# Kernel tuning notes

Measured on AMD Instinct MI355X. Metric: run time of the kernel, lower is better.

Reference implementation:

```python
import jax, jax.numpy as jnp
import numpy as np

B, T, W = 64, 64, 20
VIDEO_DIM = 1024
JOINT_DIM = 1024
K, STRIDE = 4, 4
MARGIN = 0.2
EPS = 1e-8


def _l2norm(x, axis=-1):
    n = jnp.sqrt(jnp.sum(x * x, axis=axis, keepdims=True))
    return x / jnp.maximum(n, EPS)


def _conv1d(x, w, b, stride):
    # x: (B, C, L), w: (O, I, K) -> (B, O, L_out), VALID padding (padding=0)
    y = jax.lax.conv_general_dilated(x, w, (stride,), 'VALID',
                                     dimension_numbers=('NCH', 'OIH', 'NCH'))
    return y + b[None, :, None]


def _diag_loss(scores, margin):
    # faithful port of diag(): row/column margin costs with zeroed diagonal
    b = scores.shape[0]
    d = jnp.diagonal(scores)
    off = 1.0 - jnp.eye(b, dtype=scores.dtype)
    cost_s = jnp.maximum(margin + scores - d[:, None], 0.0) * off
    cost_im = jnp.maximum(margin + scores - d[None, :], 0.0) * off
    return cost_s.sum() / b + cost_im.sum() / b


def setup_inputs() -> dict:
    key = jax.random.key(0)
    ks = jax.random.split(key, 10)
    def g(k, shape, scale=0.02):
        return jax.random.normal(k, shape, dtype=jnp.float32) * scale
    return dict(
        video=jax.random.normal(ks[0], (B, T, VIDEO_DIM), dtype=jnp.float32),
        words=jax.random.normal(ks[1], (B, W, JOINT_DIM), dtype=jnp.float32),
        w_masks=jnp.ones((B, W), dtype=jnp.int32),
        sentences=jax.random.normal(ks[2], (B, JOINT_DIM), dtype=jnp.float32),
        conv0_w=g(ks[3], (JOINT_DIM, VIDEO_DIM, K)),
        conv0_b=jnp.zeros((JOINT_DIM,), jnp.float32),
        conv1_w=g(ks[4], (JOINT_DIM, JOINT_DIM, K)),
        conv1_b=jnp.zeros((JOINT_DIM,), jnp.float32),
        conv2_w=g(ks[5], (JOINT_DIM, JOINT_DIM, K)),
        conv2_b=jnp.zeros((JOINT_DIM,), jnp.float32),
        conv1d_w=g(ks[6], (JOINT_DIM, JOINT_DIM, 1)),
        conv1d_b=jnp.zeros((JOINT_DIM,), jnp.float32),
        fc_w=g(ks[7], (JOINT_DIM, JOINT_DIM)),
        fc_b=jnp.zeros((JOINT_DIM,), jnp.float32),
    )


def reference(video, words, w_masks, sentences,
              conv0_w, conv0_b, conv1_w, conv1_b, conv2_w, conv2_b,
              conv1d_w, conv1d_b, fc_w, fc_b):
    # Vectorizes the original per-sample python loop over the pair axes (i=sentence, j=video).
    x = jnp.transpose(video, (0, 2, 1))          # (B, C, T)
    wmask = (w_masks > 0)                        # (B, W)
    conv_params = [(conv0_w, conv0_b), (conv1_w, conv1_b), (conv2_w, conv2_b)]
    sims = []
    v_tmp = x
    for cw, cb in conv_params:
        v_tmp = jax.nn.relu(_conv1d(v_tmp, cw, cb, STRIDE))
        v = jnp.transpose(_conv1d(v_tmp, conv1d_w, conv1d_b, 1), (0, 2, 1))  # (B, Tl, D)
        # frame_by_word: masked softmax attention of frames over words
        att = jnp.einsum('jtd,iwd->ijtw', v, words)            # (i, j, Tl, W)
        att = jnp.where(wmask[:, None, None, :], att, -1e30)
        att = jax.nn.softmax(att, axis=-1)
        v_s = jnp.einsum('ijtw,iwd->ijtd', att, words)         # attended word ctx
        # cosine sim of l2-normed vectors == dot product
        sim = jnp.einsum('jtd,ijtd->ijt', _l2norm(v), _l2norm(v_s))
        sims.append(sim)
    score_all = jnp.concatenate(sims, axis=2)    # (B, B, T_total=21)
    # torch code sorts descending then means over dim 1 -> mean is sort-invariant
    scores = score_all.mean(axis=2)              # (B, B) local scores
    positive_map = score_all[jnp.arange(B), jnp.arange(B)]     # (B, T_total)
    # global branch: final conv output has length 1 -> squeeze
    g_v = _l2norm(v_tmp[:, :, 0] @ fc_w.T + fc_b)              # (B, D), unit norm
    g_scores = _l2norm(sentences) @ g_v.T                      # [i, j] = cos(g_v[j], sent[i])
    loss = _diag_loss(scores, MARGIN) + _diag_loss(g_scores, MARGIN)
    return loss, positive_map
```

## Files before the change

### kernel.cpp

```cpp
#include <hip/hip_runtime.h>
#include <cmath>
#include <cstdint>


typedef __bf16 bf16_t;
typedef bf16_t bf16x8 __attribute__((ext_vector_type(8)));
typedef bf16_t bf16x4 __attribute__((ext_vector_type(4)));
typedef float  f32x4  __attribute__((ext_vector_type(4)));

__device__ __forceinline__ void gload_lds16(const void* g, void* l) {
    __builtin_amdgcn_global_load_lds(
        (const __attribute__((address_space(1))) void*)g,
        (__attribute__((address_space(3))) void*)l, 16, 0, 0);
}

__device__ __forceinline__ int swz(int r, int c) { return (r * 8 + (c ^ (r & 7))) * 8; }

__device__ __forceinline__ int remap1(int gm) {
    if (gm < 1024) return (gm >> 4) * 21 + (gm & 15);
    if (gm < 1280) { int g = gm - 1024; return (g >> 2) * 21 + 16 + (g & 3); }
    return (gm - 1280) * 21 + 20;
}

__global__ void prep_kernel(
    const float* __restrict__ c0w, const float* __restrict__ c1w,
    const float* __restrict__ c2w,
    bf16_t* __restrict__ WT0, bf16_t* __restrict__ WT1, bf16_t* __restrict__ WT2,
    const float* __restrict__ video, bf16_t* __restrict__ Vb,
    const float* __restrict__ words, bf16_t* __restrict__ Wordsb,
    const float* __restrict__ c1dw, bf16_t* __restrict__ C1b,
    const float* __restrict__ fcw, bf16_t* __restrict__ Fb)
{
    int bx = blockIdx.x;
    if (bx < 12288) {
        const float* w; bf16_t* wt;
        if (bx < 4096)      { w = c0w; wt = WT0; }
        else if (bx < 8192) { w = c1w; wt = WT1; bx -= 4096; }
        else                { w = c2w; wt = WT2; bx -= 8192; }
        int idx = bx * 256 + threadIdx.x;
        int i = idx & 1023, o = idx >> 10;
        float4 v = *(const float4*)(w + ((size_t)o << 12) + (i << 2));
        bf16_t* base = wt + ((size_t)o << 12) + i;
        base[0]    = (bf16_t)v.x;
        base[1024] = (bf16_t)v.y;
        base[2048] = (bf16_t)v.z;
        base[3072] = (bf16_t)v.w;
    } else {
        const float* s; bf16_t* d;
        if (bx < 16384)      { s = video; d = Vb;     bx -= 12288; }
        else if (bx < 17664) { s = words; d = Wordsb; bx -= 16384; }
        else if (bx < 18688) { s = c1dw;  d = C1b;    bx -= 17664; }
        else                 { s = fcw;   d = Fb;     bx -= 18688; }
        int off = (bx * 256 + threadIdx.x) * 4;
        float4 v = *(const float4*)(s + off);
        bf16x4 o4 = { (bf16_t)v.x, (bf16_t)v.y, (bf16_t)v.z, (bf16_t)v.w };
        *(bf16x4*)(d + off) = o4;
    }
}

__global__ __launch_bounds__(256) void mgemm_kernel(
    const bf16_t* __restrict__ A, const bf16_t* __restrict__ B,
    const bf16_t* __restrict__ B2, float* __restrict__ CP,
    int N, int K, int Kchunk, int fcTile, int aRow0, int cpSlice)
{
    __shared__ __align__(16) bf16_t sA[2][4096];
    __shared__ __align__(16) bf16_t sB[2][4096];
    const int tid  = threadIdx.x;
    const int lane = tid & 63;
    const int wave = tid >> 6;
    const int bx = blockIdx.x;
    const int m0C = bx * 64;
    int m0A = m0C;
    const bf16_t* Buse = B;
    if (bx == fcTile) { m0A = aRow0; Buse = B2; }
    const int n0 = blockIdx.y * 64;
    const int k0 = blockIdx.z * Kchunk;

    const int sr = tid >> 3;
    const int pc = tid & 7;
    const int lc = pc ^ (sr & 7);
    const bf16_t* Ag = A + (size_t)(m0A + sr) * K + lc * 8;
    const bf16_t* Bg = Buse + (size_t)(n0 + sr) * K + lc * 8;
    const size_t rowskip = (size_t)32 * K;

    const int wr = (wave >> 1) * 32;
    const int wc = (wave & 1) * 32;
    const int fm = lane & 15;
    const int cb = lane >> 4;

    int offA[2][2], offB[2][2];
    #pragma unroll
    for (int h = 0; h < 2; h++) {
        offA[h][0] = swz(wr +      fm, cb + h * 4);
        offA[h][1] = swz(wr + 16 + fm, cb + h * 4);
        offB[h][0] = swz(wc +      fm, cb + h * 4);
        offB[h][1] = swz(wc + 16 + fm, cb + h * 4);
    }

    f32x4 acc[2][2];
    #pragma unroll
    for (int a = 0; a < 2; a++)
        #pragma unroll
        for (int b = 0; b < 2; b++) acc[a][b] = (f32x4){0.f, 0.f, 0.f, 0.f};

    const int nIt = Kchunk >> 6;
    {
        const bf16_t* a = Ag + k0; const bf16_t* b = Bg + k0;
        gload_lds16(a,           &sA[0][tid * 8]);
        gload_lds16(a + rowskip, &sA[0][2048 + tid * 8]);
        gload_lds16(b,           &sB[0][tid * 8]);
        gload_lds16(b + rowskip, &sB[0][2048 + tid * 8]);
    }
    for (int it = 0; it < nIt; ++it) {
        const int buf = it & 1;
        __syncthreads();
        if (it + 1 < nIt) {
            const bf16_t* a = Ag + k0 + (it + 1) * 64;
            const bf16_t* b = Bg + k0 + (it + 1) * 64;
            bf16_t* dA = &sA[buf ^ 1][0];
            bf16_t* dB = &sB[buf ^ 1][0];
            gload_lds16(a,           dA + tid * 8);
            gload_lds16(a + rowskip, dA + 2048 + tid * 8);
            gload_lds16(b,           dB + tid * 8);
            gload_lds16(b + rowskip, dB + 2048 + tid * 8);
        }
        #pragma unroll
        for (int h = 0; h < 2; h++) {
            bf16x8 a0 = *(const bf16x8*)&sA[buf][offA[h][0]];
            bf16x8 a1 = *(const bf16x8*)&sA[buf][offA[h][1]];
            bf16x8 b0 = *(const bf16x8*)&sB[buf][offB[h][0]];
            bf16x8 b1 = *(const bf16x8*)&sB[buf][offB[h][1]];
            acc[0][0] = __builtin_amdgcn_mfma_f32_16x16x32_bf16(a0, b0, acc[0][0], 0, 0, 0);
            acc[0][1] = __builtin_amdgcn_mfma_f32_16x16x32_bf16(a0, b1, acc[0][1], 0, 0, 0);
            acc[1][0] = __builtin_amdgcn_mfma_f32_16x16x32_bf16(a1, b0, acc[1][0], 0, 0, 0);
            acc[1][1] = __builtin_amdgcn_mfma_f32_16x16x32_bf16(a1, b1, acc[1][1], 0, 0, 0);
        }
    }

    float* Cz = CP + (size_t)blockIdx.z * cpSlice;
    #pragma unroll
    for (int im = 0; im < 2; im++)
        #pragma unroll
        for (int rr = 0; rr < 4; rr++) {
            int gm = m0C + wr + im * 16 + cb * 4 + rr;
            #pragma unroll
            for (int in_ = 0; in_ < 2; in_++) {
                int cg = n0 + wc + in_ * 16 + fm;
                Cz[(size_t)gm * N + cg] = acc[im][in_][rr];
            }
        }
}

__global__ void epilogueB_kernel(const float* __restrict__ CP_, int nz,
    const float* __restrict__ bias, bf16_t* __restrict__ D, int MN, int N, int relu)
{
    int idx = blockIdx.x * 256 + threadIdx.x;
    if (idx >= MN) return;
    int n = idx % N;
    float s = 0.f;
    for (int z = 0; z < nz; z++) s += CP_[(size_t)z * MN + idx];
    if (bias) s += bias[n];
    if (relu) s = fmaxf(s, 0.f);
    D[idx] = (bf16_t)s;
}

__global__ void epilogueCF_kernel(const float* __restrict__ CP_,
    const float* __restrict__ bias1, const float* __restrict__ biasf,
    bf16_t* __restrict__ VCb, float* __restrict__ GV)
{
    int idx = blockIdx.x * 256 + threadIdx.x;
    int row = idx >> 10, n = idx & 1023;
    float s = CP_[idx] + CP_[idx + 1441792] + CP_[idx + 2 * 1441792] + CP_[idx + 3 * 1441792];
    if (row < 1344) VCb[(size_t)remap1(row) * 1024 + n] = (bf16_t)(s + bias1[n]);
    else            GV[(size_t)(row - 1344) * 1024 + n] = s + biasf[n];
}

__global__ void normgram_kernel(const bf16_t* __restrict__ VCb, float* __restrict__ VN,
                                const bf16_t* __restrict__ Wb, float* __restrict__ G)
{
    int bx = blockIdx.x;
    if (bx < 1344) {
        const bf16_t* x = VCb + ((size_t)bx << 10);
        float s = 0.f;
        for (int d = threadIdx.x; d < 1024; d += 256) { float v = (float)x[d]; s += v * v; }
        #pragma unroll
        for (int o = 32; o; o >>= 1) s += __shfl_xor(s, o, 64);
        __shared__ float red[4];
        if ((threadIdx.x & 63) == 0) red[threadIdx.x >> 6] = s;
        __syncthreads();
        if (threadIdx.x == 0) VN[bx] = sqrtf(red[0] + red[1] + red[2] + red[3]);
    } else {
        int g = bx - 1344;
        int i = g / 100, piece = g % 100;
        int wave = threadIdx.x >> 6, lane = threadIdx.x & 63;
        int pair = piece * 4 + wave;
        int w = pair / 20, w2 = pair % 20;
        const bf16_t* a = Wb + (((size_t)i * 20 + w)  << 10) + lane * 16;
        const bf16_t* b = Wb + (((size_t)i * 20 + w2) << 10) + lane * 16;
        bf16x8 a0 = *(const bf16x8*)a, a1 = *(const bf16x8*)(a + 8);
        bf16x8 b0 = *(const bf16x8*)b, b1 = *(const bf16x8*)(b + 8);
        float s = 0.f;
        #pragma unroll
        for (int e = 0; e < 8; e++)
            s += (float)a0[e] * (float)b0[e] + (float)a1[e] * (float)b1[e];
        #pragma unroll
        for (int o = 32; o; o >>= 1) s += __shfl_xor(s, o, 64);
        if (lane == 0) G[(size_t)i * 400 + pair] = s;
    }
}

__global__ __launch_bounds__(256) void simscores_kernel(
    const float* __restrict__ CPat, const float* __restrict__ G_,
    const float* __restrict__ VN_, const int* __restrict__ wmask,
    float* __restrict__ SC_, float* __restrict__ out)
{
    __shared__ float Gs[400];
    __shared__ float msk[20];
    __shared__ float simbuf[1344];
    const int i = blockIdx.x;
    for (int q = threadIdx.x; q < 400; q += 256) Gs[q] = G_[(size_t)i * 400 + q];
    if (threadIdx.x < 20) msk[threadIdx.x] = (wmask[i * 20 + threadIdx.x] != 0) ? 1.f : 0.f;
    __syncthreads();

    for (int base = 0; base < 1344; base += 256) {
        int jt = base + threadIdx.x;
        if (jt < 1344) {
            float s[20], p[20];
            float mx = -1e30f;
            #pragma unroll
            for (int w = 0; w < 20; w++) {
                size_t q = (size_t)(i * 20 + w) * 1344 + jt;
                s[w] = CPat[q] + CPat[q + 1720320];
                if (msk[w] != 0.f) mx = fmaxf(mx, s[w]);
            }
            float denom = 0.f, num = 0.f;
            #pragma unroll
            for (int w = 0; w < 20; w++) {
                p[w] = (msk[w] != 0.f) ? __expf(s[w] - mx) : 0.f;
                denom += p[w];
                num   += p[w] * s[w];
            }
            float quad = 0.f;
            #pragma unroll
            for (int w = 0; w < 20; w++) {
                float c = 0.f;
                #pragma unroll
                for (int w2 = 0; w2 < 20; w2++) c += Gs[w * 20 + w2] * p[w2];
                quad += p[w] * c;
            }
            float dot = num / denom;
            float vsn = sqrtf(fmaxf(quad, 0.f)) / denom;
            float sim = dot / (fmaxf(VN_[jt], 1e-8f) * fmaxf(vsn, 1e-8f));
            simbuf[jt] = sim;
            if (jt / 21 == i) out[1 + i * 21 + (jt % 21)] = sim;
        }
    }
    __syncthreads();
    if (threadIdx.x < 64) {
        int j = threadIdx.x;
        float s = 0.f;
        #pragma unroll
        for (int t = 0; t < 21; t++) s += simbuf[j * 21 + t];
        SC_[i * 64 + j] = s * (1.0f / 21.0f);
    }
}

__global__ void gscore_kernel(const float* __restrict__ sent, const float* __restrict__ GV,
                              float* __restrict__ GS_) {
    int item = blockIdx.x * 4 + (threadIdx.x >> 6);
    int i = item >> 6, j = item & 63;
    int lane = threadIdx.x & 63;
    const float* a = sent + (size_t)i * 1024;
    const float* b = GV + (size_t)j * 1024;
    float sab = 0.f, saa = 0.f, sbb = 0.f;
    #pragma unroll
    for (int q = 0; q < 16; q++) {
        int d = lane + 64 * q;
        float av = a[d], bv = b[d];
        sab += av * bv; saa += av * av; sbb += bv * bv;
    }
    #pragma unroll
    for (int o = 32; o; o >>= 1) {
        sab += __shfl_xor(sab, o, 64);
        saa += __shfl_xor(saa, o, 64);
        sbb += __shfl_xor(sbb, o, 64);
    }
    if (lane == 0)
        GS_[item] = sab / (fmaxf(sqrtf(saa), 1e-8f) * fmaxf(sqrtf(sbb), 1e-8f));
}

__global__ void loss_kernel(const float* __restrict__ SC_, const float* __restrict__ GS_,
                            float* __restrict__ out) {
    __shared__ float d1[64], d2[64], red[4];
    int tid = threadIdx.x;
    if (tid < 64) { d1[tid] = SC_[tid * 65]; d2[tid] = GS_[tid * 65]; }
    __syncthreads();
    float acc = 0.f;
    for (int idx = tid; idx < 4096; idx += 256) {
        int i = idx >> 6, j = idx & 63;
        if (i != j) {
            float s = SC_[idx];
            acc += fmaxf(0.2f + s - d1[i], 0.f) + fmaxf(0.2f + s - d1[j], 0.f);
            float g = GS_[idx];
            acc += fmaxf(0.2f + g - d2[i], 0.f) + fmaxf(0.2f + g - d2[j], 0.f);
        }
    }
    #pragma unroll
    for (int o = 32; o; o >>= 1) acc += __shfl_xor(acc, o, 64);
    if ((tid & 63) == 0) red[tid >> 6] = acc;
    __syncthreads();
    if (tid == 0) out[0] = (red[0] + red[1] + red[2] + red[3]) * (1.0f / 64.0f);
}

extern "C" void kernel_launch(void* const* d_in, const int* in_sizes, int n_in,
                              void* d_out, int out_size, void* d_ws, size_t ws_size,
                              hipStream_t stream)
{
    const float* video     = (const float*)d_in[0];
    const float* words     = (const float*)d_in[1];
    const int*   w_masks   = (const int*)  d_in[2];
    const float* sentences = (const float*)d_in[3];
    const float* conv0_w   = (const float*)d_in[4];
    const float* conv0_b   = (const float*)d_in[5];
    const float* conv1_w   = (const float*)d_in[6];
    const float* conv1_b   = (const float*)d_in[7];
    const float* conv2_w   = (const float*)d_in[8];
    const float* conv2_b   = (const float*)d_in[9];
    const float* conv1d_w  = (const float*)d_in[10];
    const float* conv1d_b  = (const float*)d_in[11];
    const float* fc_w      = (const float*)d_in[12];
    const float* fc_b      = (const float*)d_in[13];
    float* out = (float*)d_out;
    float* ws = (float*)d_ws;

    bf16_t* WT0    = (bf16_t*)(ws + 0);
    bf16_t* WT1    = (bf16_t*)(ws + 2097152);
    bf16_t* WT2    = (bf16_t*)(ws + 4194304);
    bf16_t* Vb     = (bf16_t*)(ws + 6291456);
    bf16_t* Wordsb = (bf16_t*)(ws + 8388608);
    bf16_t* C1b    = (bf16_t*)(ws + 9043968);
    bf16_t* Fb     = (bf16_t*)(ws + 9568256);
    bf16_t* Astack = (bf16_t*)(ws + 10092544);
    bf16_t* VCb    = (bf16_t*)(ws + 10780672);
    float*  CP0    = ws + 11468800;
    float*  CP1    = ws + 15663104;
    float*  CP2    = ws + 19857408;
    float*  CPcf   = ws + 21954560;
    float*  CPat   = ws + 27721728;
    float*  VN     = ws + 31162368;
    float*  GR     = ws + 31163712;
    float*  SC     = ws + 31189312;
    float*  GV     = ws + 31193408;
    float*  GS     = ws + 31258944;

    bf16_t* A2b = Astack + 1048576;
    bf16_t* A3b = Astack + 1310720;

    dim3 blk(256);

    prep_kernel<<<19712, blk, 0, stream>>>(
        conv0_w, conv1_w, conv2_w, WT0, WT1, WT2,
        video, Vb, words, Wordsb, conv1d_w, C1b, fc_w, Fb);

    mgemm_kernel<<<dim3(16,16,4), blk, 0, stream>>>(
        Vb, WT0, nullptr, CP0, 1024, 4096, 1024, -1, 0, 1048576);
    epilogueB_kernel<<<4096, blk, 0, stream>>>(CP0, 4, conv0_b, Astack, 1048576, 1024, 1);

    mgemm_kernel<<<dim3(4,16,16), blk, 0, stream>>>(
        Astack, WT1, nullptr, CP1, 1024, 4096, 256, -1, 0, 262144);
    epilogueB_kernel<<<1024, blk, 0, stream>>>(CP1, 16, conv1_b, A2b, 262144, 1024, 1);

    mgemm_kernel<<<dim3(1,16,32), blk, 0, stream>>>(
        A2b, WT2, nullptr, CP2, 1024, 4096, 128, -1, 0, 65536);
    epilogueB_kernel<<<256, blk, 0, stream>>>(CP2, 32, conv2_b, A3b, 65536, 1024, 1);

    mgemm_kernel<<<dim3(22,16,4), blk, 0, stream>>>(
        Astack, C1b, Fb, CPcf, 1024, 1024, 256, 21, 1280, 1441792);
    epilogueCF_kernel<<<5632, blk, 0, stream>>>(CPcf, conv1d_b, fc_b, VCb, GV);

    mgemm_kernel<<<dim3(20,21,2), blk, 0, stream>>>(
        Wordsb, VCb, nullptr, CPat, 1344, 1024, 512, -1, 0, 1720320);

    normgram_kernel<<<7744, blk, 0, stream>>>(VCb, VN, Wordsb, GR);
    simscores_kernel<<<64, blk, 0, stream>>>(CPat, GR, VN, w_masks, SC, out);
    gscore_kernel<<<1024, blk, 0, stream>>>(sentences, GV, GS);
    loss_kernel<<<1, blk, 0, stream>>>(SC, GS, out);
}
```

Baseline: 253.7 us.

## Fuse attention GEMM with norm/gram, split simscores across more blocks, merge gscore

Merges the attention GEMM with the row-norm and word-gram computations into one heterogeneous launch, so the independent work overlaps and one launch is saved. The 64-block simscores kernel, which underfilled the GPU, becomes a 64x6 grid that writes per-element sims to a new buffer. A second kernel then does the per-pair means, the positive-map copy and the global cosine scores together. The cost is an extra global round trip for the sims, and the fused kernel reserves GEMM-sized shared memory even for its norm and gram blocks.

New measurement: 238.2 us. 1.06x faster.

```diff
diff --git a/kernel.cpp b/kernel.cpp
--- a/kernel.cpp
+++ b/kernel.cpp
@@ -151,6 +151,130 @@
         }
 }
 
+__global__ __launch_bounds__(256) void attn_ng_kernel(
+    const bf16_t* __restrict__ A, const bf16_t* __restrict__ B,
+    float* __restrict__ CP,
+    const bf16_t* __restrict__ VCb, float* __restrict__ VN,
+    const bf16_t* __restrict__ Wb, float* __restrict__ G)
+{
+    __shared__ __align__(16) bf16_t sA[2][4096];
+    __shared__ __align__(16) bf16_t sB[2][4096];
+    __shared__ float red[4];
+    const int bxg = blockIdx.x;
+    const int tid = threadIdx.x;
+
+    if (bxg < 840) {
+        const int z = bxg / 420;
+        const int rem = bxg - z * 420;
+        const int xt = rem % 20, yt = rem / 20;
+        const int lane = tid & 63;
+        const int wave = tid >> 6;
+        const int m0 = xt * 64, n0 = yt * 64;
+        const int k0 = z * 512;
+        const int N = 1344, K = 1024;
+
+        const int sr = tid >> 3;
+        const int pc = tid & 7;
+        const int lc = pc ^ (sr & 7);
+        const bf16_t* Ag = A + (size_t)(m0 + sr) * K + lc * 8;
+        const bf16_t* Bg = B + (size_t)(n0 + sr) * K + lc * 8;
+        const size_t rowskip = (size_t)32 * K;
+
+        const int wr = (wave >> 1) * 32;
+        const int wc = (wave & 1) * 32;
+        const int fm = lane & 15;
+        const int cb = lane >> 4;
+
+        int offA[2][2], offB[2][2];
+        #pragma unroll
+        for (int h = 0; h < 2; h++) {
+            offA[h][0] = swz(wr +      fm, cb + h * 4);
+            offA[h][1] = swz(wr + 16 + fm, cb + h * 4);
+            offB[h][0] = swz(wc +      fm, cb + h * 4);
+            offB[h][1] = swz(wc + 16 + fm, cb + h * 4);
+        }
+
+        f32x4 acc[2][2];
+        #pragma unroll
+        for (int a = 0; a < 2; a++)
+            #pragma unroll
+            for (int b = 0; b < 2; b++) acc[a][b] = (f32x4){0.f, 0.f, 0.f, 0.f};
+
+        {
+            const bf16_t* a = Ag + k0; const bf16_t* b = Bg + k0;
+            gload_lds16(a,           &sA[0][tid * 8]);
+            gload_lds16(a + rowskip, &sA[0][2048 + tid * 8]);
+            gload_lds16(b,           &sB[0][tid * 8]);
+            gload_lds16(b + rowskip, &sB[0][2048 + tid * 8]);
+        }
+        for (int it = 0; it < 8; ++it) {
+            const int buf = it & 1;
+            __syncthreads();
+            if (it + 1 < 8) {
+                const bf16_t* a = Ag + k0 + (it + 1) * 64;
+                const bf16_t* b = Bg + k0 + (it + 1) * 64;
+                bf16_t* dA = &sA[buf ^ 1][0];
+                bf16_t* dB = &sB[buf ^ 1][0];
+                gload_lds16(a,           dA + tid * 8);
+                gload_lds16(a + rowskip, dA + 2048 + tid * 8);
+                gload_lds16(b,           dB + tid * 8);
+                gload_lds16(b + rowskip, dB + 2048 + tid * 8);
+            }
+            #pragma unroll
+            for (int h = 0; h < 2; h++) {
+                bf16x8 a0 = *(const bf16x8*)&sA[buf][offA[h][0]];
+                bf16x8 a1 = *(const bf16x8*)&sA[buf][offA[h][1]];
+                bf16x8 b0 = *(const bf16x8*)&sB[buf][offB[h][0]];
+                bf16x8 b1 = *(const bf16x8*)&sB[buf][offB[h][1]];
+                acc[0][0] = __builtin_amdgcn_mfma_f32_16x16x32_bf16(a0, b0, acc[0][0], 0, 0, 0);
+                acc[0][1] = __builtin_amdgcn_mfma_f32_16x16x32_bf16(a0, b1, acc[0][1], 0, 0, 0);
+                acc[1][0] = __builtin_amdgcn_mfma_f32_16x16x32_bf16(a1, b0, acc[1][0], 0, 0, 0);
+                acc[1][1] = __builtin_amdgcn_mfma_f32_16x16x32_bf16(a1, b1, acc[1][1], 0, 0, 0);
+            }
+        }
+
+        float* Cz = CP + (size_t)z * 1720320;
+        #pragma unroll
+        for (int im = 0; im < 2; im++)
+            #pragma unroll
+            for (int rr = 0; rr < 4; rr++) {
+                int gm = m0 + wr + im * 16 + cb * 4 + rr;
+                #pragma unroll
+                for (int in_ = 0; in_ < 2; in_++) {
+                    int cg = n0 + wc + in_ * 16 + fm;
+                    Cz[(size_t)gm * N + cg] = acc[im][in_][rr];
+                }
+            }
+    } else if (bxg < 2184) {
+        int r = bxg - 840;
+        const bf16_t* x = VCb + ((size_t)r << 10);
+        float s = 0.f;
+        for (int d = tid; d < 1024; d += 256) { float v = (float)x[d]; s += v * v; }
+        #pragma unroll
+        for (int o = 32; o; o >>= 1) s += __shfl_xor(s, o, 64);
+        if ((tid & 63) == 0) red[tid >> 6] = s;
+        __syncthreads();
+        if (tid == 0) VN[r] = sqrtf(red[0] + red[1] + red[2] + red[3]);
+    } else {
+        int g = bxg - 2184;
+        int i = g / 100, piece = g % 100;
+        int wave = tid >> 6, lane = tid & 63;
+        int pair = piece * 4 + wave;
+        int w = pair / 20, w2 = pair % 20;
+        const bf16_t* a = Wb + (((size_t)i * 20 + w)  << 10) + lane * 16;
+        const bf16_t* b = Wb + (((size_t)i * 20 + w2) << 10) + lane * 16;
+        bf16x8 a0 = *(const bf16x8*)a, a1 = *(const bf16x8*)(a + 8);
+        bf16x8 b0 = *(const bf16x8*)b, b1 = *(const bf16x8*)(b + 8);
+        float s = 0.f;
+        #pragma unroll
+        for (int e = 0; e < 8; e++)
+            s += (float)a0[e] * (float)b0[e] + (float)a1[e] * (float)b1[e];
+        #pragma unroll
+        for (int o = 32; o; o >>= 1) s += __shfl_xor(s, o, 64);
+        if (lane == 0) G[(size_t)i * 400 + pair] = s;
+    }
+}
+
 __global__ void epilogueB_kernel(const float* __restrict__ CP_, int nz,
     const float* __restrict__ bias, bf16_t* __restrict__ D, int MN, int N, int relu)
 {
@@ -175,118 +299,89 @@
     else            GV[(size_t)(row - 1344) * 1024 + n] = s + biasf[n];
 }
 
-__global__ void normgram_kernel(const bf16_t* __restrict__ VCb, float* __restrict__ VN,
-                                const bf16_t* __restrict__ Wb, float* __restrict__ G)
-{
-    int bx = blockIdx.x;
-    if (bx < 1344) {
-        const bf16_t* x = VCb + ((size_t)bx << 10);
-        float s = 0.f;
-        for (int d = threadIdx.x; d < 1024; d += 256) { float v = (float)x[d]; s += v * v; }
-        #pragma unroll
-        for (int o = 32; o; o >>= 1) s += __shfl_xor(s, o, 64);
-        __shared__ float red[4];
-        if ((threadIdx.x & 63) == 0) red[threadIdx.x >> 6] = s;
-        __syncthreads();
-        if (threadIdx.x == 0) VN[bx] = sqrtf(red[0] + red[1] + red[2] + red[3]);
-    } else {
-        int g = bx - 1344;
-        int i = g / 100, piece = g % 100;
-        int wave = threadIdx.x >> 6, lane = threadIdx.x & 63;
-        int pair = piece * 4 + wave;
-        int w = pair / 20, w2 = pair % 20;
-        const bf16_t* a = Wb + (((size_t)i * 20 + w)  << 10) + lane * 16;
-        const bf16_t* b = Wb + (((size_t)i * 20 + w2) << 10) + lane * 16;
-        bf16x8 a0 = *(const bf16x8*)a, a1 = *(const bf16x8*)(a + 8);
-        bf16x8 b0 = *(const bf16x8*)b, b1 = *(const bf16x8*)(b + 8);
-        float s = 0.f;
-        #pragma unroll
-        for (int e = 0; e < 8; e++)
-            s += (float)a0[e] * (float)b0[e] + (float)a1[e] * (float)b1[e];
-        #pragma unroll
-        for (int o = 32; o; o >>= 1) s += __shfl_xor(s, o, 64);
-        if (lane == 0) G[(size_t)i * 400 + pair] = s;
-    }
-}
-
-__global__ __launch_bounds__(256) void simscores_kernel(
+__global__ __launch_bounds__(256) void sim_kernel(
     const float* __restrict__ CPat, const float* __restrict__ G_,
     const float* __restrict__ VN_, const int* __restrict__ wmask,
-    float* __restrict__ SC_, float* __restrict__ out)
+    float* __restrict__ SA_)
 {
     __shared__ float Gs[400];
     __shared__ float msk[20];
-    __shared__ float simbuf[1344];
-    const int i = blockIdx.x;
+    const int i  = blockIdx.x;
+    const int jt = blockIdx.y * 256 + threadIdx.x;
     for (int q = threadIdx.x; q < 400; q += 256) Gs[q] = G_[(size_t)i * 400 + q];
     if (threadIdx.x < 20) msk[threadIdx.x] = (wmask[i * 20 + threadIdx.x] != 0) ? 1.f : 0.f;
     __syncthreads();
-
-    for (int base = 0; base < 1344; base += 256) {
-        int jt = base + threadIdx.x;
-        if (jt < 1344) {
-            float s[20], p[20];
-            float mx = -1e30f;
+    if (jt >= 1344) return;
+
+    float s[20], p[20];
+    float mx = -1e30f;
+    #pragma unroll
+    for (int w = 0; w < 20; w++) {
+        size_t q = (size_t)(i * 20 + w) * 1344 + jt;
+        s[w] = CPat[q] + CPat[q + 1720320];
+        if (msk[w] != 0.f) mx = fmaxf(mx, s[w]);
+    }
+    float denom = 0.f, num = 0.f;
+    #pragma unroll
+    for (int w = 0; w < 20; w++) {
+        p[w] = (msk[w] != 0.f) ? __expf(s[w] - mx) : 0.f;
+        denom += p[w];
+        num   += p[w] * s[w];
+    }
+    float quad = 0.f;
+    #pragma unroll
+    for (int w = 0; w < 20; w++) {
+        float c = 0.f;
+        #pragma unroll
+        for (int w2 = 0; w2 < 20; w2++) c += Gs[w * 20 + w2] * p[w2];
+        quad += p[w] * c;
+    }
+    float dot = num / denom;
+    float vsn = sqrtf(fmaxf(quad, 0.f)) / denom;
+    float sim = dot / (fmaxf(VN_[jt], 1e-8f) * fmaxf(vsn, 1e-8f));
+    SA_[(size_t)i * 1344 + jt] = sim;
+}
+
+__global__ void sg_kernel(const float* __restrict__ SA_, float* __restrict__ SC_,
+                          float* __restrict__ out,
+                          const float* __restrict__ sent, const float* __restrict__ GV,
+                          float* __restrict__ GS_)
+{
+    int bx = blockIdx.x;
+    if (bx < 16) {
+        int idx = bx * 256 + threadIdx.x;
+        int i = idx >> 6, j = idx & 63;
+        const float* row = SA_ + (size_t)idx * 21;
+        float s = 0.f;
+        #pragma unroll
+        for (int t = 0; t < 21; t++) s += row[t];
+        SC_[idx] = s * (1.0f / 21.0f);
+        if (i == j) {
             #pragma unroll
-            for (int w = 0; w < 20; w++) {
-                size_t q = (size_t)(i * 20 + w) * 1344 + jt;
-                s[w] = CPat[q] + CPat[q + 1720320];
-                if (msk[w] != 0.f) mx = fmaxf(mx, s[w]);
-            }
-            float denom = 0.f, num = 0.f;
-            #pragma unroll
-            for (int w = 0; w < 20; w++) {
-                p[w] = (msk[w] != 0.f) ? __expf(s[w] - mx) : 0.f;
-                denom += p[w];
-                num   += p[w] * s[w];
-            }
-            float quad = 0.f;
-            #pragma unroll
-            for (int w = 0; w < 20; w++) {
-                float c = 0.f;
-                #pragma unroll
-                for (int w2 = 0; w2 < 20; w2++) c += Gs[w * 20 + w2] * p[w2];
-                quad += p[w] * c;
-            }
-            float dot = num / denom;
-            float vsn = sqrtf(fmaxf(quad, 0.f)) / denom;
-            float sim = dot / (fmaxf(VN_[jt], 1e-8f) * fmaxf(vsn, 1e-8f));
-            simbuf[jt] = sim;
-            if (jt / 21 == i) out[1 + i * 21 + (jt % 21)] = sim;
-        }
-    }
-    __syncthreads();
-    if (threadIdx.x < 64) {
-        int j = threadIdx.x;
-        float s = 0.f;
-        #pragma unroll
-        for (int t = 0; t < 21; t++) s += simbuf[j * 21 + t];
-        SC_[i * 64 + j] = s * (1.0f / 21.0f);
-    }
-}
-
-__global__ void gscore_kernel(const float* __restrict__ sent, const float* __restrict__ GV,
-                              float* __restrict__ GS_) {
-    int item = blockIdx.x * 4 + (threadIdx.x >> 6);
-    int i = item >> 6, j = item & 63;
-    int lane = threadIdx.x & 63;
-    const float* a = sent + (size_t)i * 1024;
-    const float* b = GV + (size_t)j * 1024;
-    float sab = 0.f, saa = 0.f, sbb = 0.f;
-    #pragma unroll
-    for (int q = 0; q < 16; q++) {
-        int d = lane + 64 * q;
-        float av = a[d], bv = b[d];
-        sab += av * bv; saa += av * av; sbb += bv * bv;
-    }
-    #pragma unroll
-    for (int o = 32; o; o >>= 1) {
-        sab += __shfl_xor(sab, o, 64);
-        saa += __shfl_xor(saa, o, 64);
-        sbb += __shfl_xor(sbb, o, 64);
-    }
-    if (lane == 0)
-        GS_[item] = sab / (fmaxf(sqrtf(saa), 1e-8f) * fmaxf(sqrtf(sbb), 1e-8f));
+            for (int t = 0; t < 21; t++) out[1 + i * 21 + t] = row[t];
+        }
+    } else {
+        int item = (bx - 16) * 4 + (threadIdx.x >> 6);
+        int i = item >> 6, j = item & 63;
+        int lane = threadIdx.x & 63;
+        const float* a = sent + (size_t)i * 1024;
+        const float* b = GV + (size_t)j * 1024;
+        float sab = 0.f, saa = 0.f, sbb = 0.f;
+        #pragma unroll
+        for (int q = 0; q < 16; q++) {
+            int d = lane + 64 * q;
+            float av = a[d], bv = b[d];
+            sab += av * bv; saa += av * av; sbb += bv * bv;
+        }
+        #pragma unroll
+        for (int o = 32; o; o >>= 1) {
+            sab += __shfl_xor(sab, o, 64);
+            saa += __shfl_xor(saa, o, 64);
+            sbb += __shfl_xor(sbb, o, 64);
+        }
+        if (lane == 0)
+            GS_[item] = sab / (fmaxf(sqrtf(saa), 1e-8f) * fmaxf(sqrtf(sbb), 1e-8f));
+    }
 }
 
 __global__ void loss_kernel(const float* __restrict__ SC_, const float* __restrict__ GS_,
@@ -349,9 +444,10 @@
     float*  CPat   = ws + 27721728;
     float*  VN     = ws + 31162368;
     float*  GR     = ws + 31163712;
-    float*  SC     = ws + 31189312;
-    float*  GV     = ws + 31193408;
-    float*  GS     = ws + 31258944;
+    float*  SA     = ws + 31189312;
+    float*  SC     = ws + 31275328;
+    float*  GV     = ws + 31279424;
+    float*  GS     = ws + 31344960;
 
     bf16_t* A2b = Astack + 1048576;
     bf16_t* A3b = Astack + 1310720;
@@ -378,11 +474,10 @@
         Astack, C1b, Fb, CPcf, 1024, 1024, 256, 21, 1280, 1441792);
     epilogueCF_kernel<<<5632, blk, 0, stream>>>(CPcf, conv1d_b, fc_b, VCb, GV);
 
-    mgemm_kernel<<<dim3(20,21,2), blk, 0, stream>>>(
-        Wordsb, VCb, nullptr, CPat, 1344, 1024, 512, -1, 0, 1720320);
-
-    normgram_kernel<<<7744, blk, 0, stream>>>(VCb, VN, Wordsb, GR);
-    simscores_kernel<<<64, blk, 0, stream>>>(CPat, GR, VN, w_masks, SC, out);
-    gscore_kernel<<<1024, blk, 0, stream>>>(sentences, GV, GS);
+    attn_ng_kernel<<<8584, blk, 0, stream>>>(
+        Wordsb, VCb, CPat, VCb, VN, Wordsb, GR);
+
+    sim_kernel<<<dim3(64,6), blk, 0, stream>>>(CPat, GR, VN, w_masks, SA);
+    sg_kernel<<<1040, blk, 0, stream>>>(SA, SC, out, sentences, GV, GS);
     loss_kernel<<<1, blk, 0, stream>>>(SC, GS, out);
 }
```
